# Kernel tuning notes

Measured on AMD Instinct MI355X. Metric: run time of the kernel, lower is better.

The kernel has to match this reference:

```python
import jax, jax.numpy as jnp
import numpy as np

N = 50000       # nodes
E = 1250000     # edges
DIM = 64
H = 16
DPH = DIM // H  # 4
LN_EPS = 1e-5


def setup_inputs() -> dict:
    key = jax.random.key(0)
    ks = jax.random.split(key, 10)
    return {
        "node_feat": jax.random.normal(ks[0], (N, DIM), jnp.float32),
        "edge_feat": jax.random.normal(ks[1], (E, H, DPH), jnp.float32),
        "node_vec": jax.random.normal(ks[2], (N, 3, DIM), jnp.float32),
        "radial": jax.random.uniform(ks[3], (E,), jnp.float32),
        "ln_g": jnp.ones((DIM,), jnp.float32),
        "ln_b": jnp.zeros((DIM,), jnp.float32),
        "qkv_w": jax.random.normal(ks[4], (DIM, 3 * DIM), jnp.float32) / np.sqrt(DIM).astype(np.float32),
        "qkv_b": jnp.zeros((3 * DIM,), jnp.float32),
        "vec_w": jax.random.normal(ks[5], (DIM, 2 * DIM), jnp.float32) / np.sqrt(DIM).astype(np.float32),
        "out_w": jax.random.normal(ks[6], (DIM, 2 * DIM), jnp.float32) / np.sqrt(DIM).astype(np.float32),
        "out_b": jnp.zeros((2 * DIM,), jnp.float32),
        "row": jax.random.randint(ks[7], (E,), 0, N, jnp.int32),
        "col": jax.random.randint(ks[8], (E,), 0, N, jnp.int32),
        "natoms": N,
    }


def reference(node_feat, edge_feat, node_vec, radial, ln_g, ln_b,
              qkv_w, qkv_b, vec_w, out_w, out_b, row, col, natoms):
    # LayerNorm (biased variance, as torch)
    mu = jnp.mean(node_feat, axis=-1, keepdims=True)
    var = jnp.mean(jnp.square(node_feat - mu), axis=-1, keepdims=True)
    x = (node_feat - mu) * jax.lax.rsqrt(var + LN_EPS) * ln_g + ln_b

    # QKV projection -> [N, H, 3*DPH], split
    qkv = (x @ qkv_w + qkv_b).reshape(-1, H, 3 * DPH)
    q = qkv[..., :DPH]
    k = qkv[..., DPH:2 * DPH]
    v = qkv[..., 2 * DPH:]

    # Gather by edge indices, gated dot-product attention per edge  [E, H]
    attn = jax.nn.gelu(jnp.sum(q[row] * k[col], axis=-1), approximate=False) * radial[:, None]

    # Equivariant vector gate  [N, DIM]
    iv = node_vec @ vec_w  # [N, 3, 2*DIM]
    input_dot = jnp.sum(iv[..., :DIM] * iv[..., DIM:], axis=-2)

    # Edge messages and scatter-add into nodes
    m = v[col] * edge_feat * attn[..., None]          # [E, H, DPH]
    m_agg = jax.ops.segment_sum(m, row, num_segments=natoms)  # [N, H, DPH]
    m_agg = m_agg.reshape(natoms, DIM)

    out = m_agg @ out_w + out_b                        # [N, 2*DIM]
    return input_dot * out[..., :DIM] + out[..., DIM:]
```

## Files before the change

### kernel.cpp

```cpp
#include <hip/hip_runtime.h>
#include <math.h>

#define DIM 64
#define NW 4
#define NPB 4

__device__ __forceinline__ float waveReduceSum(float v) {
    #pragma unroll
    for (int off = 1; off < 64; off <<= 1)
        v += __shfl_xor(v, off, 64);
    return v;
}

__global__ __launch_bounds__(256) void qkv_kernel(
    const float* __restrict__ node_feat,
    const float* __restrict__ ln_g, const float* __restrict__ ln_b,
    const float* __restrict__ qkv_w, const float* __restrict__ qkv_b,
    float* __restrict__ q, float* __restrict__ k, float* __restrict__ v,
    int N)
{
    __shared__ float  wlds[64 * 192];
    __shared__ float4 xs[NW][NPB][16];
    const int wave = threadIdx.x >> 6, lane = threadIdx.x & 63;

    for (int idx = threadIdx.x; idx < 64 * 192; idx += 256) {
        int d = idx / 192, j = idx - d * 192;
        int jj = j & 63, sec = j >> 6;
        int c = 12 * (jj >> 2) + (jj & 3) + 4 * sec;
        wlds[idx] = qkv_w[d * 192 + c];
    }
    const int c0 = 12 * (lane >> 2) + (lane & 3);
    const float b0 = qkv_b[c0], b1 = qkv_b[c0 + 4], b2 = qkv_b[c0 + 8];
    const float gg = ln_g[lane], bb = ln_b[lane];
    __syncthreads();

    const int nstride = gridDim.x * NW * NPB;
    for (int n0 = (blockIdx.x * NW + wave) * NPB; n0 < N; n0 += nstride) {
        const int cnt = min(NPB, N - n0);
        float acc0[NPB], acc1[NPB], acc2[NPB];
        #pragma unroll
        for (int i = 0; i < NPB; ++i) {
            acc0[i] = b0; acc1[i] = b1; acc2[i] = b2;
            if (i < cnt) {
                float nf = node_feat[(size_t)(n0 + i) * DIM + lane];
                float mu = waveReduceSum(nf) * (1.0f / 64.0f);
                float dv = nf - mu;
                float var = waveReduceSum(dv * dv) * (1.0f / 64.0f);
                float x = dv * rsqrtf(var + 1e-5f) * gg + bb;
                ((float*)&xs[wave][i][0])[lane] = x;
            }
        }
        #pragma unroll 4
        for (int d4 = 0; d4 < 16; ++d4) {
            float4 xv[NPB];
            #pragma unroll
            for (int i = 0; i < NPB; ++i) xv[i] = xs[wave][i][d4];
            #pragma unroll
            for (int u = 0; u < 4; ++u) {
                int d = d4 * 4 + u;
                float w0 = wlds[d * 192 + lane];
                float w1 = wlds[d * 192 + lane + 64];
                float w2 = wlds[d * 192 + lane + 128];
                #pragma unroll
                for (int i = 0; i < NPB; ++i) {
                    float xd = (&xv[i].x)[u];
                    acc0[i] = fmaf(xd, w0, acc0[i]);
                    acc1[i] = fmaf(xd, w1, acc1[i]);
                    acc2[i] = fmaf(xd, w2, acc2[i]);
                }
            }
        }
        #pragma unroll
        for (int i = 0; i < NPB; ++i) if (i < cnt) {
            size_t off = (size_t)(n0 + i) * DIM + lane;
            q[off] = acc0[i]; k[off] = acc1[i]; v[off] = acc2[i];
        }
    }
}

__global__ __launch_bounds__(256) void vec_kernel(
    const float* __restrict__ node_vec,
    const float* __restrict__ vec_w,
    float* __restrict__ input_dot,
    float* __restrict__ m_agg,
    int N)
{
    __shared__ float  vlds[64 * 128];
    __shared__ float4 nvs[NW][NPB][3][16];
    const int wave = threadIdx.x >> 6, lane = threadIdx.x & 63;

    for (int idx = threadIdx.x; idx < 64 * 128; idx += 256)
        vlds[idx] = vec_w[idx];
    __syncthreads();

    const int nstride = gridDim.x * NW * NPB;
    for (int n0 = (blockIdx.x * NW + wave) * NPB; n0 < N; n0 += nstride) {
        const int cnt = min(NPB, N - n0);
        float a0[NPB][3], a1[NPB][3];
        #pragma unroll
        for (int i = 0; i < NPB; ++i) {
            #pragma unroll
            for (int s = 0; s < 3; ++s) {
                a0[i][s] = 0.f; a1[i][s] = 0.f;
                if (i < cnt)
                    ((float*)&nvs[wave][i][s][0])[lane] =
                        node_vec[((size_t)(n0 + i) * 3 + s) * DIM + lane];
            }
        }
        #pragma unroll 2
        for (int d4 = 0; d4 < 16; ++d4) {
            #pragma unroll
            for (int u = 0; u < 4; ++u) {
                int d = d4 * 4 + u;
                float w0 = vlds[d * 128 + lane];
                float w1 = vlds[d * 128 + lane + 64];
                #pragma unroll
                for (int i = 0; i < NPB; ++i) {
                    #pragma unroll
                    for (int s = 0; s < 3; ++s) {
                        float nv = ((float*)&nvs[wave][i][s][d4])[u];
                        a0[i][s] = fmaf(nv, w0, a0[i][s]);
                        a1[i][s] = fmaf(nv, w1, a1[i][s]);
                    }
                }
            }
        }
        #pragma unroll
        for (int i = 0; i < NPB; ++i) if (i < cnt) {
            size_t off = (size_t)(n0 + i) * DIM + lane;
            input_dot[off] = a0[i][0] * a1[i][0] + a0[i][1] * a1[i][1]
                           + a0[i][2] * a1[i][2];
            m_agg[off] = 0.0f;
        }
    }
}

__global__ __launch_bounds__(256) void edge_kernel(
    const float* __restrict__ q,
    const float* __restrict__ k,
    const float* __restrict__ v,
    const float* __restrict__ edge_feat,
    const float* __restrict__ radial,
    const int* __restrict__ row,
    const int* __restrict__ col,
    float* __restrict__ m_agg,
    int E)
{
    const int wave = threadIdx.x >> 6, lane = threadIdx.x & 63;
    const int e = blockIdx.x * NW + wave;
    if (e >= E) return;

    const int r = row[e];
    const int c = col[e];

    float qd = q[(size_t)r * DIM + lane];
    float kd = k[(size_t)c * DIM + lane];
    float p = qd * kd;
    p += __shfl_xor(p, 1, 64);
    p += __shfl_xor(p, 2, 64);

    float g = 0.5f * p * (1.0f + erff(p * 0.70710678118654752f));
    float a = g * radial[e];

    float ef = __builtin_nontemporal_load(&edge_feat[(size_t)e * DIM + lane]);
    float m = v[(size_t)c * DIM + lane] * ef * a;
    atomicAdd(&m_agg[(size_t)r * DIM + lane], m);
}

__global__ __launch_bounds__(256) void out_kernel(
    const float* __restrict__ m_agg,
    const float* __restrict__ input_dot,
    const float* __restrict__ out_w,
    const float* __restrict__ out_b,
    float* __restrict__ result,
    int N)
{
    __shared__ float  olds[64 * 128];
    __shared__ float4 ms[NW][NPB][16];
    const int wave = threadIdx.x >> 6, lane = threadIdx.x & 63;

    for (int idx = threadIdx.x; idx < 64 * 128; idx += 256)
        olds[idx] = out_w[idx];
    const float ob0 = out_b[lane], ob1 = out_b[lane + 64];
    __syncthreads();

    const int nstride = gridDim.x * NW * NPB;
    for (int n0 = (blockIdx.x * NW + wave) * NPB; n0 < N; n0 += nstride) {
        const int cnt = min(NPB, N - n0);
        float o0[NPB], o1[NPB];
        #pragma unroll
        for (int i = 0; i < NPB; ++i) {
            o0[i] = ob0; o1[i] = ob1;
            if (i < cnt)
                ((float*)&ms[wave][i][0])[lane] =
                    m_agg[(size_t)(n0 + i) * DIM + lane];
        }
        #pragma unroll 4
        for (int d4 = 0; d4 < 16; ++d4) {
            float4 mv[NPB];
            #pragma unroll
            for (int i = 0; i < NPB; ++i) mv[i] = ms[wave][i][d4];
            #pragma unroll
            for (int u = 0; u < 4; ++u) {
                int d = d4 * 4 + u;
                float w0 = olds[d * 128 + lane];
                float w1 = olds[d * 128 + lane + 64];
                #pragma unroll
                for (int i = 0; i < NPB; ++i) {
                    float md = (&mv[i].x)[u];
                    o0[i] = fmaf(md, w0, o0[i]);
                    o1[i] = fmaf(md, w1, o1[i]);
                }
            }
        }
        #pragma unroll
        for (int i = 0; i < NPB; ++i) if (i < cnt) {
            size_t off = (size_t)(n0 + i) * DIM + lane;
            result[off] = input_dot[off] * o0[i] + o1[i];
        }
    }
}

extern "C" void kernel_launch(void* const* d_in, const int* in_sizes, int n_in,
                              void* d_out, int out_size, void* d_ws, size_t ws_size,
                              hipStream_t stream)
{
    const float* node_feat = (const float*)d_in[0];
    const float* edge_feat = (const float*)d_in[1];
    const float* node_vec  = (const float*)d_in[2];
    const float* radial    = (const float*)d_in[3];
    const float* ln_g      = (const float*)d_in[4];
    const float* ln_b      = (const float*)d_in[5];
    const float* qkv_w     = (const float*)d_in[6];
    const float* qkv_b     = (const float*)d_in[7];
    const float* vec_w     = (const float*)d_in[8];
    const float* out_w     = (const float*)d_in[9];
    const float* out_b     = (const float*)d_in[10];
    const int*   row       = (const int*)d_in[11];
    const int*   col       = (const int*)d_in[12];

    const int N = in_sizes[0] / DIM;
    const int E = in_sizes[3];

    float* ws    = (float*)d_ws;
    float* q     = ws;
    float* k     = q    + (size_t)N * DIM;
    float* v     = k    + (size_t)N * DIM;
    float* idot  = v    + (size_t)N * DIM;
    float* m_agg = idot + (size_t)N * DIM;

    const int grid_nodes = 768;
    const int eblk = (E + NW - 1) / NW;

    qkv_kernel<<<grid_nodes, 256, 0, stream>>>(node_feat, ln_g, ln_b,
                                               qkv_w, qkv_b, q, k, v, N);
    vec_kernel<<<grid_nodes, 256, 0, stream>>>(node_vec, vec_w, idot, m_agg, N);
    edge_kernel<<<eblk, 256, 0, stream>>>(q, k, v, edge_feat, radial,
                                          row, col, m_agg, E);
    out_kernel<<<grid_nodes, 256, 0, stream>>>(m_agg, idot, out_w, out_b,
                                               (float*)d_out, N);
}
```

Before: 859.0 us.

## Replace atomic scatter-add with CSR-by-row gather fused into output projection

Builds a per-call CSR index of edges grouped by destination row using a histogram, a single-block scan and an atomic scatter. A fused kernel then has one wave per node walk its edges, accumulate messages in registers and apply the output projection directly. This removes the per-edge float atomics and the m_agg round trip. In exchange it adds three preprocessing kernels, a serial one-block scan, and edge_feat reads that are no longer coalesced because edges are accessed in permuted order.

```diff
diff --git a/kernel.cpp b/kernel.cpp
--- a/kernel.cpp
+++ b/kernel.cpp
@@ -82,7 +82,6 @@
     const float* __restrict__ node_vec,
     const float* __restrict__ vec_w,
     float* __restrict__ input_dot,
-    float* __restrict__ m_agg,
     int N)
 {
     __shared__ float  vlds[64 * 128];
@@ -130,45 +129,62 @@
             size_t off = (size_t)(n0 + i) * DIM + lane;
             input_dot[off] = a0[i][0] * a1[i][0] + a0[i][1] * a1[i][1]
                            + a0[i][2] * a1[i][2];
-            m_agg[off] = 0.0f;
-        }
-    }
-}
-
-__global__ __launch_bounds__(256) void edge_kernel(
+        }
+    }
+}
+
+__global__ __launch_bounds__(256) void hist_kernel(
+    const int* __restrict__ row, int* __restrict__ cnt, int E)
+{
+    int i = blockIdx.x * 256 + threadIdx.x;
+    if (i < E) atomicAdd(&cnt[row[i]], 1);
+}
+
+__global__ __launch_bounds__(1024) void scan_kernel(
+    const int* __restrict__ cnt, int* __restrict__ off,
+    int* __restrict__ cursor, int N)
+{
+    __shared__ int ls[1024];
+    const int t = threadIdx.x;
+    const int per = (N + 1023) / 1024;
+    const int s0 = t * per, s1 = min(s0 + per, N);
+    int sum = 0;
+    for (int i = s0; i < s1; ++i) sum += cnt[i];
+    ls[t] = sum;
+    __syncthreads();
+    for (int d = 1; d < 1024; d <<= 1) {
+        int val = (t >= d) ? ls[t - d] : 0;
+        __syncthreads();
+        if (t >= d) ls[t] += val;
+        __syncthreads();
+    }
+    int run = (t > 0) ? ls[t - 1] : 0;
+    for (int i = s0; i < s1; ++i) {
+        off[i] = run; cursor[i] = run; run += cnt[i];
+    }
+    if (t == 1023) off[N] = ls[1023];
+}
+
+__global__ __launch_bounds__(256) void scatter_kernel(
+    const int* __restrict__ row, int* __restrict__ cursor,
+    int* __restrict__ eid, int E)
+{
+    int i = blockIdx.x * 256 + threadIdx.x;
+    if (i < E) {
+        int pos = atomicAdd(&cursor[row[i]], 1);
+        eid[pos] = i;
+    }
+}
+
+__global__ __launch_bounds__(256) void agg_out_kernel(
     const float* __restrict__ q,
     const float* __restrict__ k,
     const float* __restrict__ v,
     const float* __restrict__ edge_feat,
     const float* __restrict__ radial,
-    const int* __restrict__ row,
     const int* __restrict__ col,
-    float* __restrict__ m_agg,
-    int E)
-{
-    const int wave = threadIdx.x >> 6, lane = threadIdx.x & 63;
-    const int e = blockIdx.x * NW + wave;
-    if (e >= E) return;
-
-    const int r = row[e];
-    const int c = col[e];
-
-    float qd = q[(size_t)r * DIM + lane];
-    float kd = k[(size_t)c * DIM + lane];
-    float p = qd * kd;
-    p += __shfl_xor(p, 1, 64);
-    p += __shfl_xor(p, 2, 64);
-
-    float g = 0.5f * p * (1.0f + erff(p * 0.70710678118654752f));
-    float a = g * radial[e];
-
-    float ef = __builtin_nontemporal_load(&edge_feat[(size_t)e * DIM + lane]);
-    float m = v[(size_t)c * DIM + lane] * ef * a;
-    atomicAdd(&m_agg[(size_t)r * DIM + lane], m);
-}
-
-__global__ __launch_bounds__(256) void out_kernel(
-    const float* __restrict__ m_agg,
+    const int* __restrict__ off,
+    const int* __restrict__ eid,
     const float* __restrict__ input_dot,
     const float* __restrict__ out_w,
     const float* __restrict__ out_b,
@@ -176,7 +192,7 @@
     int N)
 {
     __shared__ float  olds[64 * 128];
-    __shared__ float4 ms[NW][NPB][16];
+    __shared__ float4 ms[NW][16];
     const int wave = threadIdx.x >> 6, lane = threadIdx.x & 63;
 
     for (int idx = threadIdx.x; idx < 64 * 128; idx += 256)
@@ -184,40 +200,70 @@
     const float ob0 = out_b[lane], ob1 = out_b[lane + 64];
     __syncthreads();
 
-    const int nstride = gridDim.x * NW * NPB;
-    for (int n0 = (blockIdx.x * NW + wave) * NPB; n0 < N; n0 += nstride) {
-        const int cnt = min(NPB, N - n0);
-        float o0[NPB], o1[NPB];
-        #pragma unroll
-        for (int i = 0; i < NPB; ++i) {
-            o0[i] = ob0; o1[i] = ob1;
-            if (i < cnt)
-                ((float*)&ms[wave][i][0])[lane] =
-                    m_agg[(size_t)(n0 + i) * DIM + lane];
-        }
+    const float inv_sqrt2 = 0.70710678118654752f;
+    const int wstride = gridDim.x * NW;
+    for (int n = blockIdx.x * NW + wave; n < N; n += wstride) {
+        const float qv = q[(size_t)n * DIM + lane];
+        float acc = 0.f;
+        const int start = off[n], end = off[n + 1];
+
+        for (int j0 = start; j0 < end; j0 += 64) {
+            const int m = min(64, end - j0);
+            int e = 0, c = 0; float rad = 0.f;
+            if (lane < m) {
+                e = eid[j0 + lane];
+                c = col[e];
+                rad = radial[e];
+            }
+            int i = 0;
+            for (; i + 2 <= m; i += 2) {
+                int   e0 = __shfl(e, i, 64),     e1 = __shfl(e, i + 1, 64);
+                int   c0 = __shfl(c, i, 64),     c1 = __shfl(c, i + 1, 64);
+                float r0 = __shfl(rad, i, 64),   r1 = __shfl(rad, i + 1, 64);
+                float k0 = k[(size_t)c0 * DIM + lane];
+                float k1 = k[(size_t)c1 * DIM + lane];
+                float v0 = v[(size_t)c0 * DIM + lane];
+                float v1 = v[(size_t)c1 * DIM + lane];
+                float f0 = __builtin_nontemporal_load(&edge_feat[(size_t)e0 * DIM + lane]);
+                float f1 = __builtin_nontemporal_load(&edge_feat[(size_t)e1 * DIM + lane]);
+                float p0 = qv * k0;
+                p0 += __shfl_xor(p0, 1, 64); p0 += __shfl_xor(p0, 2, 64);
+                float p1 = qv * k1;
+                p1 += __shfl_xor(p1, 1, 64); p1 += __shfl_xor(p1, 2, 64);
+                float g0 = 0.5f * p0 * (1.0f + erff(p0 * inv_sqrt2)) * r0;
+                float g1 = 0.5f * p1 * (1.0f + erff(p1 * inv_sqrt2)) * r1;
+                acc = fmaf(v0 * f0, g0, acc);
+                acc = fmaf(v1 * f1, g1, acc);
+            }
+            for (; i < m; ++i) {
+                int   e0 = __shfl(e, i, 64);
+                int   c0 = __shfl(c, i, 64);
+                float r0 = __shfl(rad, i, 64);
+                float k0 = k[(size_t)c0 * DIM + lane];
+                float v0 = v[(size_t)c0 * DIM + lane];
+                float f0 = __builtin_nontemporal_load(&edge_feat[(size_t)e0 * DIM + lane]);
+                float p0 = qv * k0;
+                p0 += __shfl_xor(p0, 1, 64); p0 += __shfl_xor(p0, 2, 64);
+                float g0 = 0.5f * p0 * (1.0f + erff(p0 * inv_sqrt2)) * r0;
+                acc = fmaf(v0 * f0, g0, acc);
+            }
+        }
+
+        ((float*)&ms[wave][0])[lane] = acc;
+        float o0 = ob0, o1 = ob1;
         #pragma unroll 4
         for (int d4 = 0; d4 < 16; ++d4) {
-            float4 mv[NPB];
-            #pragma unroll
-            for (int i = 0; i < NPB; ++i) mv[i] = ms[wave][i][d4];
+            float4 mv = ms[wave][d4];
             #pragma unroll
             for (int u = 0; u < 4; ++u) {
                 int d = d4 * 4 + u;
-                float w0 = olds[d * 128 + lane];
-                float w1 = olds[d * 128 + lane + 64];
-                #pragma unroll
-                for (int i = 0; i < NPB; ++i) {
-                    float md = (&mv[i].x)[u];
-                    o0[i] = fmaf(md, w0, o0[i]);
-                    o1[i] = fmaf(md, w1, o1[i]);
-                }
-            }
-        }
-        #pragma unroll
-        for (int i = 0; i < NPB; ++i) if (i < cnt) {
-            size_t off = (size_t)(n0 + i) * DIM + lane;
-            result[off] = input_dot[off] * o0[i] + o1[i];
-        }
+                float md = (&mv.x)[u];
+                o0 = fmaf(md, olds[d * 128 + lane], o0);
+                o1 = fmaf(md, olds[d * 128 + lane + 64], o1);
+            }
+        }
+        size_t offr = (size_t)n * DIM + lane;
+        result[offr] = input_dot[offr] * o0 + o1;
     }
 }
 
@@ -242,21 +288,26 @@
     const int N = in_sizes[0] / DIM;
     const int E = in_sizes[3];
 
-    float* ws    = (float*)d_ws;
-    float* q     = ws;
-    float* k     = q    + (size_t)N * DIM;
-    float* v     = k    + (size_t)N * DIM;
-    float* idot  = v    + (size_t)N * DIM;
-    float* m_agg = idot + (size_t)N * DIM;
+    float* q    = (float*)d_ws;
+    float* k    = q    + (size_t)N * DIM;
+    float* v    = k    + (size_t)N * DIM;
+    float* idot = v    + (size_t)N * DIM;
+    int* eid    = (int*)(idot + (size_t)N * DIM);
+    int* cnt    = eid + E;
+    int* off    = cnt + N;
+    int* cursor = off + N + 1;
 
     const int grid_nodes = 768;
-    const int eblk = (E + NW - 1) / NW;
-
+    const int eblk = (E + 255) / 256;
+
+    hipMemsetAsync(cnt, 0, (size_t)N * sizeof(int), stream);
     qkv_kernel<<<grid_nodes, 256, 0, stream>>>(node_feat, ln_g, ln_b,
                                                qkv_w, qkv_b, q, k, v, N);
-    vec_kernel<<<grid_nodes, 256, 0, stream>>>(node_vec, vec_w, idot, m_agg, N);
-    edge_kernel<<<eblk, 256, 0, stream>>>(q, k, v, edge_feat, radial,
-                                          row, col, m_agg, E);
-    out_kernel<<<grid_nodes, 256, 0, stream>>>(m_agg, idot, out_w, out_b,
-                                               (float*)d_out, N);
-}
+    vec_kernel<<<grid_nodes, 256, 0, stream>>>(node_vec, vec_w, idot, N);
+    hist_kernel<<<eblk, 256, 0, stream>>>(row, cnt, E);
+    scan_kernel<<<1, 1024, 0, stream>>>(cnt, off, cursor, N);
+    scatter_kernel<<<eblk, 256, 0, stream>>>(row, cursor, eid, E);
+    agg_out_kernel<<<3072, 256, 0, stream>>>(q, k, v, edge_feat, radial,
+                                             col, off, eid, idot,
+                                             out_w, out_b, (float*)d_out, N);
+}
```

Result: slower. 939.8 us (+9.4%).
